# Performance work log

Hardware: AMD Instinct MI355X
Metric: run time of the kernel (lower is better)

## Reference

```python
import jax, jax.numpy as jnp
import numpy as np

D_MODEL = 1024
H = 16
D_K = D_MODEL // H  # 64


def setup_inputs() -> dict:
    key = jax.random.key(0)
    ks = jax.random.split(key, 10)
    s = 1.0 / np.sqrt(D_MODEL)
    x = jax.random.normal(ks[0], (4, 2048, D_MODEL), dtype=jnp.float32)
    # Per-head linear weights stacked: [H, d_model, d_k]
    Wq = jax.random.uniform(ks[1], (H, D_MODEL, D_K), jnp.float32, -s, s)
    bq = jax.random.uniform(ks[2], (H, D_K), jnp.float32, -s, s)
    Wk = jax.random.uniform(ks[3], (H, D_MODEL, D_K), jnp.float32, -s, s)
    bk = jax.random.uniform(ks[4], (H, D_K), jnp.float32, -s, s)
    Wv = jax.random.uniform(ks[5], (H, D_MODEL, D_K), jnp.float32, -s, s)
    bv = jax.random.uniform(ks[6], (H, D_K), jnp.float32, -s, s)
    so = 1.0 / np.sqrt(H * D_K)
    Wo = jax.random.uniform(ks[7], (H * D_K, D_MODEL), jnp.float32, -so, so)
    bo = jax.random.uniform(ks[8], (D_MODEL,), jnp.float32, -so, so)
    return {"x": x, "Wq": Wq, "bq": bq, "Wk": Wk, "bk": bk, "Wv": Wv, "bv": bv, "Wo": Wo, "bo": bo}


def reference(x, Wq, bq, Wk, bk, Wv, bv, Wo, bo):
    # x: [B, S, D]; Wq/Wk/Wv: [H, D, d_k]; b*: [H, d_k]
    q = jnp.einsum('bsd,hdk->bhsk', x, Wq) + bq[None, :, None, :]
    k = jnp.einsum('bsd,hdk->bhsk', x, Wk) + bk[None, :, None, :]
    v = jnp.einsum('bsd,hdk->bhsk', x, Wv) + bv[None, :, None, :]
    scores = jnp.einsum('bhqk,bhsk->bhqs', q, k) / np.sqrt(D_K)
    S = x.shape[1]
    causal = jnp.triu(jnp.ones((S, S), dtype=bool), k=1)  # True above diagonal
    scores = jnp.where(causal, -jnp.inf, scores)
    attn = jax.nn.softmax(scores, axis=-1)
    ctx = jnp.einsum('bhqs,bhsk->bhqk', attn, v)  # [B, H, S, d_k]
    B = x.shape[0]
    # concat heads: torch cats head outputs along last dim -> [B, S, H*d_k]
    ctx = jnp.transpose(ctx, (0, 2, 1, 3)).reshape(B, S, H * D_K)
    return ctx @ Wo + bo
```

## Files before the change

### kernel.cpp

```cpp
#include <hip/hip_runtime.h>
#include <hip/hip_bf16.h>

typedef unsigned short u16;
typedef __attribute__((ext_vector_type(8))) short short8;
typedef __attribute__((ext_vector_type(4))) short short4v;
typedef __attribute__((ext_vector_type(4))) float floatx4;

#define D_MODEL 1024
#define NH 16
#define SEQ 2048
#define BATCH 4
#define M_ROWS 8192
#define N_QKV 3072
#define PS_LD 72

#define QSCALE 0.18033688011112042f
#define EXP2_OFF 11.541560327111707f

__device__ __forceinline__ u16 f2u(float f) {
    __hip_bfloat16 h = __float2bfloat16(f);
    u16 u; __builtin_memcpy(&u, &h, 2); return u;
}

__device__ __forceinline__ void async_copy16(const u16* g, u16* l) {
    __builtin_amdgcn_global_load_lds(
        (const __attribute__((address_space(1))) unsigned int*)(g),
        (__attribute__((address_space(3))) unsigned int*)(l),
        16, 0, 0);
}

__global__ __launch_bounds__(256) void prep(
    const float* __restrict__ x,
    const float* __restrict__ Wq, const float* __restrict__ Wk,
    const float* __restrict__ Wv, const float* __restrict__ Wo,
    const float* __restrict__ bq, const float* __restrict__ bk,
    const float* __restrict__ bv, const float* __restrict__ bo,
    u16* __restrict__ xb, u16* __restrict__ Wpt, u16* __restrict__ Wot,
    float* __restrict__ biasp)
{
    __shared__ u16 T[64 * 72];
    const int tid = threadIdx.x;
    const int blk = blockIdx.x;

    if (blk < 4096) {
        size_t i = ((size_t)blk * 256 + tid) * 8;
        float4 f0 = *(const float4*)&x[i];
        float4 f1 = *(const float4*)&x[i + 4];
        u16 t[8] = {f2u(f0.x), f2u(f0.y), f2u(f0.z), f2u(f0.w),
                    f2u(f1.x), f2u(f1.y), f2u(f1.z), f2u(f1.w)};
        *(short8*)&xb[i] = *(short8*)t;
        return;
    }
    if (blk == 5120) {
        #pragma unroll
        for (int j = 0; j < 16; j++) {
            int idx = j * 256 + tid;
            float v;
            if (idx < 1024)      v = bq[idx] * QSCALE;
            else if (idx < 2048) v = bk[idx - 1024];
            else if (idx < 3072) v = bv[idx - 2048];
            else                 v = bo[idx - 3072];
            biasp[idx] = v;
        }
        return;
    }
    const int wb = blk - 4096;
    const int r = tid >> 2, s4 = (tid & 3) * 16;
    if (wb < 768) {
        int sel = wb / 256, rem = wb % 256;
        int h = rem >> 4, ktile = rem & 15;
        const float* W = (sel == 0) ? Wq : ((sel == 1) ? Wk : Wv);
        const float scale = (sel == 0) ? QSCALE : 1.0f;
        const float* src = W + ((size_t)h * 1024 + ktile * 64 + r) * 64 + s4;
        #pragma unroll
        for (int i = 0; i < 16; i++) T[(s4 + i) * 72 + r] = f2u(src[i] * scale);
        __syncthreads();
        u16 tmp[16];
        #pragma unroll
        for (int i = 0; i < 16; i++) tmp[i] = T[r * 72 + s4 + i];
        u16* dst = Wpt + ((size_t)sel * 1024 + h * 64 + r) * 1024 + ktile * 64 + s4;
        *(short8*)&dst[0] = *(short8*)&tmp[0];
        *(short8*)&dst[8] = *(short8*)&tmp[8];
    } else {
        int rem = wb - 768;
        int nt = rem >> 4, kt2 = rem & 15;
        const float* src = Wo + ((size_t)kt2 * 64 + r) * 1024 + nt * 64 + s4;
        #pragma unroll
        for (int i = 0; i < 16; i++) T[(s4 + i) * 72 + r] = f2u(src[i]);
        __syncthreads();
        u16 tmp[16];
        #pragma unroll
        for (int i = 0; i < 16; i++) tmp[i] = T[r * 72 + s4 + i];
        u16* dst = Wot + ((size_t)nt * 64 + r) * 1024 + kt2 * 64 + s4;
        *(short8*)&dst[0] = *(short8*)&tmp[0];
        *(short8*)&dst[8] = *(short8*)&tmp[8];
    }
}

__global__ __launch_bounds__(256) void vtrans(const u16* __restrict__ QKV,
                                              u16* __restrict__ Vtg) {
    __shared__ u16 T[64 * 72];
    const int bh = blockIdx.x, kt = blockIdx.y;
    const int b = bh >> 4, h = bh & 15;
    const int tid = threadIdx.x;
    const int r = tid >> 2, s4 = (tid & 3) * 16;
    const u16* vp = QKV + (size_t)(b * SEQ + kt * 64 + r) * N_QKV + 2 * D_MODEL + h * 64 + s4;
    *(short8*)&T[r * 72 + s4]     = *(const short8*)&vp[0];
    *(short8*)&T[r * 72 + s4 + 8] = *(const short8*)&vp[8];
    __syncthreads();
    u16 tmp[16];
    #pragma unroll
    for (int i = 0; i < 16; i++) tmp[i] = T[(s4 + i) * 72 + r];
    u16* op = Vtg + ((size_t)bh * 64 + r) * SEQ + kt * 64 + s4;
    *(short8*)&op[0] = *(short8*)&tmp[0];
    *(short8*)&op[8] = *(short8*)&tmp[8];
}

template <typename OT>
__global__ __launch_bounds__(256) void gemm128(
    const u16* __restrict__ A, const u16* __restrict__ Bt,
    const float* __restrict__ bias, OT* __restrict__ C,
    int M, int N, int K)
{
    __shared__ u16 As[128 * 64];
    __shared__ u16 Bs[128 * 64];
    const int tid = threadIdx.x;
    const int w = tid >> 6, lane = tid & 63;
    const int l16 = lane & 15, quad = lane >> 4;

    const int nwgx = gridDim.x;
    const int nwg = nwgx * gridDim.y;
    const int lin = blockIdx.y * nwgx + blockIdx.x;
    const int cpx = nwg >> 3;
    const int swz = (lin & 7) * cpx + (lin >> 3);
    const int bn = (swz % nwgx) * 128, bm = (swz / nwgx) * 128;

    const int wr = (w >> 1) * 64, wc = (w & 1) * 64;

    floatx4 acc[4][4];
    #pragma unroll
    for (int i = 0; i < 4; i++)
        #pragma unroll
        for (int j = 0; j < 4; j++) acc[i][j] = (floatx4){0.f, 0.f, 0.f, 0.f};

    for (int k0 = 0; k0 < K; k0 += 64) {
        #pragma unroll
        for (int c = 0; c < 4; c++) {
            const int off = (w * 4 + c) * 1024 + lane * 16;
            const int row = off >> 7, seg = (off >> 4) & 7;
            async_copy16(A  + (size_t)(bm + row) * K + k0 + seg * 8, &As[(w * 4 + c) * 512]);
            async_copy16(Bt + (size_t)(bn + row) * K + k0 + seg * 8, &Bs[(w * 4 + c) * 512]);
        }
        __syncthreads();
        #pragma unroll
        for (int kc = 0; kc < 2; kc++) {
            short8 a[4], b[4];
            #pragma unroll
            for (int i = 0; i < 4; i++)
                a[i] = *(short8*)&As[(wr + i * 16 + l16) * 64 + kc * 32 + quad * 8];
            #pragma unroll
            for (int i = 0; i < 4; i++)
                b[i] = *(short8*)&Bs[(wc + i * 16 + l16) * 64 + kc * 32 + quad * 8];
            #pragma unroll
            for (int mm = 0; mm < 4; mm++)
                #pragma unroll
                for (int nn = 0; nn < 4; nn++)
                    acc[mm][nn] = __builtin_amdgcn_mfma_f32_16x16x32_bf16(
                        a[mm], b[nn], acc[mm][nn], 0, 0, 0);
        }
        __syncthreads();
    }

    #pragma unroll
    for (int nn = 0; nn < 4; nn++) {
        const int col = bn + wc + nn * 16 + l16;
        const float bi = bias[col];
        #pragma unroll
        for (int mm = 0; mm < 4; mm++) {
            const int row = bm + wr + mm * 16 + quad * 4;
            #pragma unroll
            for (int r = 0; r < 4; r++) {
                float v = acc[mm][nn][r] + bi;
                if constexpr (sizeof(OT) == 2) ((u16*)C)[(size_t)(row + r) * N + col] = f2u(v);
                else                           C[(size_t)(row + r) * N + col] = v;
            }
        }
    }
}

#define G256_BAR   __builtin_amdgcn_s_barrier()
#define G256_LGKM(n) { asm volatile("s_waitcnt lgkmcnt(" #n ")" ::: "memory"); \
                       __builtin_amdgcn_sched_barrier(0); }

#define GQ_STAGE_A(bb, ca, kq) \
    async_copy16(pAc + (size_t)(ca) * 64 * K + (kq), \
                 &lds[(bb) * 28672 + (ca) * 4096 + stw]);

#define GQ_STAGE_B(bb, cb, kq) \
    async_copy16(pBc + (size_t)(cb) * 64 * K + (kq), \
                 &lds[(bb) * 28672 + 16384 + (cb) * 4096 + stw]);

#define GQ_LDA4(dst, bb, mi0) { \
    const int _b = (bb) * 28672 + wm * 8192; \
    _Pragma("unroll") \
    for (int mi = 0; mi < 4; mi++) { \
        const int _r = _b + (((mi0) + mi) * 16 + l16) * 64; \
        dst[mi * 2]     = *(const short8*)&lds[_r + col0]; \
        dst[mi * 2 + 1] = *(const short8*)&lds[_r + col1]; \
    } }

#define GQ_LDB2(dst, bb, ni0) { \
    const int _b = (bb) * 28672 + 16384 + wn * 3072; \
    _Pragma("unroll") \
    for (int ni = 0; ni < 2; ni++) { \
        const int _r = _b + (((ni0) + ni) * 16 + l16) * 64; \
        dst[ni * 2]     = *(const short8*)&lds[_r + col0]; \
        dst[ni * 2 + 1] = *(const short8*)&lds[_r + col1]; \
    } }

#define GQ_LDB1(dst, bb, ni0) { \
    const int _b = (bb) * 28672 + 16384 + wn * 3072; \
    const int _r = _b + ((ni0) * 16 + l16) * 64; \
    dst[0] = *(const short8*)&lds[_r + col0]; \
    dst[1] = *(const short8*)&lds[_r + col1]; }

#define GQ_MMA8(av, bv, MI0, NI0) { \
    _Pragma("unroll") \
    for (int mi = 0; mi < 4; mi++) \
    _Pragma("unroll") \
    for (int ni = 0; ni < 2; ni++) { \
        acc[(MI0) + mi][(NI0) + ni] = __builtin_amdgcn_mfma_f32_16x16x32_bf16( \
            bv[ni * 2],     av[mi * 2],     acc[(MI0) + mi][(NI0) + ni], 0, 0, 0); \
        acc[(MI0) + mi][(NI0) + ni] = __builtin_amdgcn_mfma_f32_16x16x32_bf16( \
            bv[ni * 2 + 1], av[mi * 2 + 1], acc[(MI0) + mi][(NI0) + ni], 0, 0, 0); \
    } }

#define GQ_MMA4(av, bv, MI0) { \
    _Pragma("unroll") \
    for (int mi = 0; mi < 4; mi++) { \
        acc[(MI0) + mi][2] = __builtin_amdgcn_mfma_f32_16x16x32_bf16( \
            bv[0], av[mi * 2],     acc[(MI0) + mi][2], 0, 0, 0); \
        acc[(MI0) + mi][2] = __builtin_amdgcn_mfma_f32_16x16x32_bf16( \
            bv[1], av[mi * 2 + 1], acc[(MI0) + mi][2], 0, 0, 0); \
    } }

template <typename OT>
__global__ __launch_bounds__(512, 2) void gemm_qkv(
    const u16* __restrict__ A, const u16* __restrict__ Bt,
    const float* __restrict__ bias, OT* __restrict__ C,
    int M, int N, int K)
{
    __shared__ u16 lds[57344];
    const int tid = threadIdx.x;
    const int w = tid >> 6, lane = tid & 63;
    const int l16 = lane & 15, quad = lane >> 4;
    const int wm = w >> 2, wn = w & 3;

    const int nwgx = gridDim.x;
    const int nwg = nwgx * gridDim.y;
    const int lin = blockIdx.y * nwgx + blockIdx.x;
    const int cpx = nwg >> 3;
    const int swz = (lin & 7) * cpx + (lin >> 3);
    const int bn = (swz % nwgx) * 192, bm = (swz / nwgx) * 256;

    const int d = tid * 16;
    const int s = d ^ (((d >> 7) & 7) << 4);
    const int r = s >> 7;
    const int c = (s & 127) >> 1;
    const u16* pAc = A  + (size_t)(bm + r) * K + c;
    const u16* pBc = Bt + (size_t)(bn + r) * K + c;
    const int stw = w * 512;

    const int xm = (l16 & 7) << 3;
    const int col0 = (quad * 8) ^ xm;
    const int col1 = (32 + quad * 8) ^ xm;

    floatx4 acc[8][3];
    #pragma unroll
    for (int i = 0; i < 8; i++)
        #pragma unroll
        for (int j = 0; j < 3; j++) acc[i][j] = (floatx4){0.f, 0.f, 0.f, 0.f};

    GQ_STAGE_A(0, 0, 0); GQ_STAGE_A(0, 1, 0); GQ_STAGE_A(0, 2, 0); GQ_STAGE_A(0, 3, 0);
    GQ_STAGE_B(0, 0, 0); GQ_STAGE_B(0, 1, 0); GQ_STAGE_B(0, 2, 0);
    GQ_STAGE_B(1, 0, 64); GQ_STAGE_B(1, 1, 64); GQ_STAGE_B(1, 2, 64);
    asm volatile("s_waitcnt vmcnt(3)" ::: "memory");
    __syncthreads();

    short8 a0[8], a1[8], b0[4], b1[2];
    GQ_LDA4(a0, 0, 0);
    GQ_LDB2(b0, 0, 0);

    const int NKT = K >> 6;
    for (int kt = 0; kt < NKT; ++kt) {
        const int buf = kt & 1, nb = buf ^ 1;
        const int kqA = (kt + 1) << 6, kqB = (kt + 2) << 6;
        const bool st1 = (kt + 1 < NKT), st2 = (kt + 2 < NKT);

        GQ_LDB1(b1, buf, 2);
        if (st1) { GQ_STAGE_A(nb, 0, kqA); GQ_STAGE_A(nb, 1, kqA); }
        G256_BAR; G256_LGKM(2);
        __builtin_amdgcn_s_setprio(1); GQ_MMA8(a0, b0, 0, 0);
        __builtin_amdgcn_s_setprio(0); G256_BAR;

        GQ_LDA4(a1, buf, 4);
        if (st1) { GQ_STAGE_A(nb, 2, kqA); GQ_STAGE_A(nb, 3, kqA); }
        G256_BAR; G256_LGKM(8);
        __builtin_amdgcn_s_setprio(1); GQ_MMA4(a0, b1, 0);
        __builtin_amdgcn_s_setprio(0); G256_BAR;

        if (st2) { GQ_STAGE_B(buf, 0, kqB); GQ_STAGE_B(buf, 1, kqB); }
        G256_BAR; G256_LGKM(0);
        __builtin_amdgcn_s_setprio(1); GQ_MMA8(a1, b0, 4, 0);
        __builtin_amdgcn_s_setprio(0); G256_BAR;

        if (st2) { GQ_STAGE_B(buf, 2, kqB); }
        if (st1) {
            if (st2) { asm volatile("s_waitcnt vmcnt(3)" ::: "memory"); }
            else     { asm volatile("s_waitcnt vmcnt(0)" ::: "memory"); }
            __builtin_amdgcn_sched_barrier(0);
            GQ_LDA4(a0, nb, 0);
            GQ_LDB2(b0, nb, 0);
        }
        G256_BAR;
        __builtin_amdgcn_s_setprio(1); GQ_MMA4(a1, b1, 4);
        __builtin_amdgcn_s_setprio(0); G256_BAR;
    }

    float4 bi[3];
    #pragma unroll
    for (int ni = 0; ni < 3; ni++)
        bi[ni] = *(const float4*)&bias[bn + wn * 48 + ni * 16 + quad * 4];
    #pragma unroll
    for (int mi = 0; mi < 8; mi++) {
        const int row = bm + wm * 128 + mi * 16 + l16;
        #pragma unroll
        for (int ni = 0; ni < 3; ni++) {
            const int col = bn + wn * 48 + ni * 16 + quad * 4;
            const float v0 = acc[mi][ni][0] + bi[ni].x;
            const float v1 = acc[mi][ni][1] + bi[ni].y;
            const float v2 = acc[mi][ni][2] + bi[ni].z;
            const float v3 = acc[mi][ni][3] + bi[ni].w;
            if constexpr (sizeof(OT) == 2) {
                u16 o[4] = {f2u(v0), f2u(v1), f2u(v2), f2u(v3)};
                *(short4v*)&((u16*)C)[(size_t)row * N + col] = *(short4v*)o;
            } else {
                float4 fv = {v0, v1, v2, v3};
                *(float4*)&C[(size_t)row * N + col] = fv;
            }
        }
    }
}

__global__ __launch_bounds__(256) void attn_mfma(
    const u16* __restrict__ QKV, const u16* __restrict__ Vtg, u16* __restrict__ ctx)
{
    __shared__ u16 Ks[2][64 * 64];
    __shared__ u16 Vs[2][64 * 64];
    __shared__ u16 Ps[128 * PS_LD];

    const int bh = blockIdx.x;
    const int qt = (int)(gridDim.y - 1) - (int)blockIdx.y;
    const int b = bh >> 4, h = bh & 15;
    const int tid = threadIdx.x;
    const int w = tid >> 6, lane = tid & 63;
    const int l16 = lane & 15, quad = lane >> 4;

    const int r0 = tid >> 3,        c0 = tid & 7;
    const int r1 = (256 + tid) >> 3, c1 = tid & 7;
    const int sw0 = c0 ^ (r0 & 7), sw1 = c1 ^ (r1 & 7);

    short8 q[2][2];
    #pragma unroll
    for (int m = 0; m < 2; m++) {
        const u16* qp = QKV + (size_t)(b * SEQ + qt * 128 + w * 32 + m * 16 + l16) * N_QKV + h * 64;
        q[m][0] = *(const short8*)&qp[quad * 8];
        q[m][1] = *(const short8*)&qp[32 + quad * 8];
    }

    short8 ones8;
    #pragma unroll
    for (int i = 0; i < 8; i++) ones8[i] = (short)0x3F80;

    floatx4 O[2][4];
    floatx4 lsum[2];
    #pragma unroll
    for (int m = 0; m < 2; m++) {
        lsum[m] = (floatx4){0.f, 0.f, 0.f, 0.f};
        #pragma unroll
        for (int i = 0; i < 4; i++) O[m][i] = (floatx4){0.f, 0.f, 0.f, 0.f};
    }

    const int nkt = 2 * qt + 2;
    const int qrow_w_max = qt * 128 + w * 32 + 31;

    const size_t kbase = (size_t)(b * SEQ) * N_QKV + D_MODEL + h * 64;
    const size_t vbase = (size_t)bh * 64 * SEQ;

    const u16* kpa = QKV + kbase + (size_t)r0 * N_QKV + c0 * 8;
    const u16* kpb = QKV + kbase + (size_t)r1 * N_QKV + c1 * 8;
    const u16* vpa = Vtg + vbase + (size_t)r0 * SEQ + c0 * 8;
    const u16* vpb = Vtg + vbase + (size_t)r1 * SEQ + c1 * 8;

    {
        float4 ka = *(const float4*)kpa;
        float4 kb = *(const float4*)kpb;
        float4 va = *(const float4*)vpa;
        float4 vb = *(const float4*)vpb;
        *(float4*)&Ks[0][r0 * 64 + sw0 * 8] = ka;
        *(float4*)&Ks[0][r1 * 64 + sw1 * 8] = kb;
        *(float4*)&Vs[0][r0 * 64 + sw0 * 8] = va;
        *(float4*)&Vs[0][r1 * 64 + sw1 * 8] = vb;
    }
    kpa += (size_t)64 * N_QKV; kpb += (size_t)64 * N_QKV;
    vpa += 64; vpb += 64;
    __syncthreads();

    for (int kt = 0; kt < nkt; kt++) {
        const int buf = kt & 1;
        const bool pre = (kt + 1 < nkt);
        float4 ka, kb, va, vb;
        if (pre) {
            ka = *(const float4*)kpa;
            kb = *(const float4*)kpb;
            va = *(const float4*)vpa;
            vb = *(const float4*)vpb;
            kpa += (size_t)64 * N_QKV; kpb += (size_t)64 * N_QKV;
            vpa += 64; vpb += 64;
        }

        if (kt * 64 <= qrow_w_max) {
            short8 kf[4][2];
            #pragma unroll
            for (int ns = 0; ns < 4; ns++) {
                const int rr = ns * 16 + l16, rs = rr & 7;
                kf[ns][0] = *(short8*)&Ks[buf][rr * 64 + (quad ^ rs) * 8];
                kf[ns][1] = *(short8*)&Ks[buf][rr * 64 + ((4 + quad) ^ rs) * 8];
            }
            const bool needMask = (kt * 64 + 63 > qt * 128 + w * 32);

            #pragma unroll
            for (int m = 0; m < 2; m++) {
                floatx4 z[4];
                __builtin_amdgcn_s_setprio(1);
                #pragma unroll
                for (int ns = 0; ns < 4; ns++) {
                    floatx4 t = (floatx4){0.f, 0.f, 0.f, 0.f};
                    t = __builtin_amdgcn_mfma_f32_16x16x32_bf16(kf[ns][0], q[m][0], t, 0, 0, 0);
                    t = __builtin_amdgcn_mfma_f32_16x16x32_bf16(kf[ns][1], q[m][1], t, 0, 0, 0);
                    z[ns] = t;
                }
                __builtin_amdgcn_s_setprio(0);
                const int qrow_g = qt * 128 + w * 32 + m * 16 + l16;
                const int prow = (w * 32 + m * 16 + l16) * PS_LD;
                #pragma unroll
                for (int ns = 0; ns < 4; ns++) {
                    u16 pk[4];
                    #pragma unroll
                    for (int r = 0; r < 4; r++) {
                        float s = z[ns][r];
                        const int key = kt * 64 + ns * 16 + quad * 4 + r;
                        if (needMask && key > qrow_g) s = -INFINITY;
                        float p = __builtin_amdgcn_exp2f(s - EXP2_OFF);
                        pk[r] = f2u(p);
                    }
                    *(short4v*)&Ps[prow + ns * 16 + quad * 4] = *(short4v*)pk;
                }
            }

            short8 vf[4][2];
            #pragma unroll
            for (int ds = 0; ds < 4; ds++) {
                const int rr = ds * 16 + l16, rs = rr & 7;
                vf[ds][0] = *(short8*)&Vs[buf][rr * 64 + (quad ^ rs) * 8];
                vf[ds][1] = *(short8*)&Vs[buf][rr * 64 + ((4 + quad) ^ rs) * 8];
            }
            __builtin_amdgcn_s_setprio(1);
            #pragma unroll
            for (int m = 0; m < 2; m++) {
                const int prow = (w * 32 + m * 16 + l16) * PS_LD;
                short8 p0 = *(short8*)&Ps[prow + quad * 8];
                short8 p1 = *(short8*)&Ps[prow + 32 + quad * 8];
                lsum[m] = __builtin_amdgcn_mfma_f32_16x16x32_bf16(ones8, p0, lsum[m], 0, 0, 0);
                lsum[m] = __builtin_amdgcn_mfma_f32_16x16x32_bf16(ones8, p1, lsum[m], 0, 0, 0);
                #pragma unroll
                for (int ds = 0; ds < 4; ds++) {
                    O[m][ds] = __builtin_amdgcn_mfma_f32_16x16x32_bf16(vf[ds][0], p0, O[m][ds], 0, 0, 0);
                    O[m][ds] = __builtin_amdgcn_mfma_f32_16x16x32_bf16(vf[ds][1], p1, O[m][ds], 0, 0, 0);
                }
            }
            __builtin_amdgcn_s_setprio(0);
        }

        if (pre) {
            const int nb = buf ^ 1;
            *(float4*)&Ks[nb][r0 * 64 + sw0 * 8] = ka;
            *(float4*)&Ks[nb][r1 * 64 + sw1 * 8] = kb;
            *(float4*)&Vs[nb][r0 * 64 + sw0 * 8] = va;
            *(float4*)&Vs[nb][r1 * 64 + sw1 * 8] = vb;
        }
        __syncthreads();
    }

    #pragma unroll
    for (int m = 0; m < 2; m++) {
        const float inv = 1.0f / lsum[m][0];
        const size_t base = (size_t)(b * SEQ + qt * 128 + w * 32 + m * 16 + l16) * D_MODEL + h * 64;
        #pragma unroll
        for (int ds = 0; ds < 4; ds++) {
            u16 o[4];
            #pragma unroll
            for (int r = 0; r < 4; r++) o[r] = f2u(O[m][ds][r] * inv);
            *(short4v*)&ctx[base + ds * 16 + quad * 4] = *(short4v*)o;
        }
    }
}

extern "C" void kernel_launch(void* const* d_in, const int* in_sizes, int n_in,
                              void* d_out, int out_size, void* d_ws, size_t ws_size,
                              hipStream_t stream) {
    const float* x  = (const float*)d_in[0];
    const float* Wq = (const float*)d_in[1];
    const float* bq = (const float*)d_in[2];
    const float* Wk = (const float*)d_in[3];
    const float* bk = (const float*)d_in[4];
    const float* Wv = (const float*)d_in[5];
    const float* bv = (const float*)d_in[6];
    const float* Wo = (const float*)d_in[7];
    const float* bo = (const float*)d_in[8];
    float* out = (float*)d_out;

    char* ws = (char*)d_ws;
    float* biasp = (float*)ws;
    u16*   Wpt   = (u16*)(ws + 0x10000);
    u16*   Wot   = (u16*)(ws + 0x620000);
    u16*   xb    = (u16*)(ws + 0x840000);
    u16*   Vtg   = xb;
    u16*   QKV   = (u16*)(ws + 0x1840000);
    u16*   ctx   = (u16*)(ws + 0x4840000);

    prep<<<5121, 256, 0, stream>>>(x, Wq, Wk, Wv, Wo, bq, bk, bv, bo,
                                   xb, Wpt, Wot, biasp);

    gemm_qkv<u16><<<dim3(N_QKV / 192, M_ROWS / 256), 512, 0, stream>>>(
        xb, Wpt, biasp, QKV, M_ROWS, N_QKV, D_MODEL);

    vtrans<<<dim3(64, 32), 256, 0, stream>>>(QKV, Vtg);

    attn_mfma<<<dim3(BATCH * NH, SEQ / 128), 256, 0, stream>>>(QKV, Vtg, ctx);

    gemm128<float><<<dim3(D_MODEL / 128, M_ROWS / 128), 256, 0, stream>>>(
        ctx, Wot, biasp + N_QKV, out, M_ROWS, D_MODEL, D_MODEL);
}
```

Before: 273.7 us.

## Pipeline output GEMM with swizzled double buffer; shrink attention P staging

Replaces the simple output-projection GEMM with a 256x128-tile, 512-thread kernel. It uses XOR-swizzled LDS, double-buffered async global-to-LDS loads and interleaved MFMA phases with priority hints, so loads overlap compute. In attention, all QK^T MFMAs for a tile are issued first. The P staging is then cut to a per-wave 16x64 swizzled LDS buffer reused across the two row groups, which lowers LDS use and allows more waves per CU (launch bounds 4). This adds scheduling complexity and relies on correct vmcnt/lgkmcnt waits for correctness.

Result: slower. 446.1 us (+63.0%).

```diff
diff --git a/kernel.cpp b/kernel.cpp
--- a/kernel.cpp
+++ b/kernel.cpp
@@ -12,7 +12,6 @@
 #define BATCH 4
 #define M_ROWS 8192
 #define N_QKV 3072
-#define PS_LD 72
 
 #define QSCALE 0.18033688011112042f
 #define EXP2_OFF 11.541560327111707f
@@ -114,78 +113,6 @@
     u16* op = Vtg + ((size_t)bh * 64 + r) * SEQ + kt * 64 + s4;
     *(short8*)&op[0] = *(short8*)&tmp[0];
     *(short8*)&op[8] = *(short8*)&tmp[8];
-}
-
-template <typename OT>
-__global__ __launch_bounds__(256) void gemm128(
-    const u16* __restrict__ A, const u16* __restrict__ Bt,
-    const float* __restrict__ bias, OT* __restrict__ C,
-    int M, int N, int K)
-{
-    __shared__ u16 As[128 * 64];
-    __shared__ u16 Bs[128 * 64];
-    const int tid = threadIdx.x;
-    const int w = tid >> 6, lane = tid & 63;
-    const int l16 = lane & 15, quad = lane >> 4;
-
-    const int nwgx = gridDim.x;
-    const int nwg = nwgx * gridDim.y;
-    const int lin = blockIdx.y * nwgx + blockIdx.x;
-    const int cpx = nwg >> 3;
-    const int swz = (lin & 7) * cpx + (lin >> 3);
-    const int bn = (swz % nwgx) * 128, bm = (swz / nwgx) * 128;
-
-    const int wr = (w >> 1) * 64, wc = (w & 1) * 64;
-
-    floatx4 acc[4][4];
-    #pragma unroll
-    for (int i = 0; i < 4; i++)
-        #pragma unroll
-        for (int j = 0; j < 4; j++) acc[i][j] = (floatx4){0.f, 0.f, 0.f, 0.f};
-
-    for (int k0 = 0; k0 < K; k0 += 64) {
-        #pragma unroll
-        for (int c = 0; c < 4; c++) {
-            const int off = (w * 4 + c) * 1024 + lane * 16;
-            const int row = off >> 7, seg = (off >> 4) & 7;
-            async_copy16(A  + (size_t)(bm + row) * K + k0 + seg * 8, &As[(w * 4 + c) * 512]);
-            async_copy16(Bt + (size_t)(bn + row) * K + k0 + seg * 8, &Bs[(w * 4 + c) * 512]);
-        }
-        __syncthreads();
-        #pragma unroll
-        for (int kc = 0; kc < 2; kc++) {
-            short8 a[4], b[4];
-            #pragma unroll
-            for (int i = 0; i < 4; i++)
-                a[i] = *(short8*)&As[(wr + i * 16 + l16) * 64 + kc * 32 + quad * 8];
-            #pragma unroll
-            for (int i = 0; i < 4; i++)
-                b[i] = *(short8*)&Bs[(wc + i * 16 + l16) * 64 + kc * 32 + quad * 8];
-            #pragma unroll
-            for (int mm = 0; mm < 4; mm++)
-                #pragma unroll
-                for (int nn = 0; nn < 4; nn++)
-                    acc[mm][nn] = __builtin_amdgcn_mfma_f32_16x16x32_bf16(
-                        a[mm], b[nn], acc[mm][nn], 0, 0, 0);
-        }
-        __syncthreads();
-    }
-
-    #pragma unroll
-    for (int nn = 0; nn < 4; nn++) {
-        const int col = bn + wc + nn * 16 + l16;
-        const float bi = bias[col];
-        #pragma unroll
-        for (int mm = 0; mm < 4; mm++) {
-            const int row = bm + wr + mm * 16 + quad * 4;
-            #pragma unroll
-            for (int r = 0; r < 4; r++) {
-                float v = acc[mm][nn][r] + bi;
-                if constexpr (sizeof(OT) == 2) ((u16*)C)[(size_t)(row + r) * N + col] = f2u(v);
-                else                           C[(size_t)(row + r) * N + col] = v;
-            }
-        }
-    }
 }
 
 #define G256_BAR   __builtin_amdgcn_s_barrier()
@@ -352,12 +279,142 @@
     }
 }
 
-__global__ __launch_bounds__(256) void attn_mfma(
+#define GO_STAGE_A(bb, ca, kq) \
+    async_copy16(pAc + (size_t)(ca) * 64 * K + (kq), \
+                 &lds[(bb) * 24576 + (ca) * 4096 + stw]);
+
+#define GO_STAGE_B(bb, cb, kq) \
+    async_copy16(pBc + (size_t)(cb) * 64 * K + (kq), \
+                 &lds[(bb) * 24576 + 16384 + (cb) * 4096 + stw]);
+
+#define GO_LDA4(dst, bb, mi0) { \
+    const int _b = (bb) * 24576 + wm * 8192; \
+    _Pragma("unroll") \
+    for (int mi = 0; mi < 4; mi++) { \
+        const int _r = _b + (((mi0) + mi) * 16 + l16) * 64; \
+        dst[mi * 2]     = *(const short8*)&lds[_r + col0]; \
+        dst[mi * 2 + 1] = *(const short8*)&lds[_r + col1]; \
+    } }
+
+#define GO_LDB1(dst, bb, ni) { \
+    const int _b = (bb) * 24576 + 16384; \
+    const int _r = _b + (wn * 32 + (ni) * 16 + l16) * 64; \
+    dst[0] = *(const short8*)&lds[_r + col0]; \
+    dst[1] = *(const short8*)&lds[_r + col1]; }
+
+#define GO_MMA(av, bv, MI0, NI) { \
+    _Pragma("unroll") \
+    for (int mi = 0; mi < 4; mi++) { \
+        acc[(MI0) + mi][NI] = __builtin_amdgcn_mfma_f32_16x16x32_bf16( \
+            bv[0], av[mi * 2],     acc[(MI0) + mi][NI], 0, 0, 0); \
+        acc[(MI0) + mi][NI] = __builtin_amdgcn_mfma_f32_16x16x32_bf16( \
+            bv[1], av[mi * 2 + 1], acc[(MI0) + mi][NI], 0, 0, 0); \
+    } }
+
+__global__ __launch_bounds__(512, 2) void gemm_out(
+    const u16* __restrict__ A, const u16* __restrict__ Bt,
+    const float* __restrict__ bias, float* __restrict__ C,
+    int M, int N, int K)
+{
+    __shared__ u16 lds[49152];
+    const int tid = threadIdx.x;
+    const int w = tid >> 6, lane = tid & 63;
+    const int l16 = lane & 15, quad = lane >> 4;
+    const int wm = w >> 2, wn = w & 3;
+
+    const int nwgx = gridDim.x;
+    const int nwg = nwgx * gridDim.y;
+    const int lin = blockIdx.y * nwgx + blockIdx.x;
+    const int cpx = nwg >> 3;
+    const int swz = (lin & 7) * cpx + (lin >> 3);
+    const int bn = (swz % nwgx) * 128, bm = (swz / nwgx) * 256;
+
+    const int d = tid * 16;
+    const int s = d ^ (((d >> 7) & 7) << 4);
+    const int r = s >> 7;
+    const int c = (s & 127) >> 1;
+    const u16* pAc = A  + (size_t)(bm + r) * K + c;
+    const u16* pBc = Bt + (size_t)(bn + r) * K + c;
+    const int stw = w * 512;
+
+    const int xm = (l16 & 7) << 3;
+    const int col0 = (quad * 8) ^ xm;
+    const int col1 = (32 + quad * 8) ^ xm;
+
+    floatx4 acc[8][2];
+    #pragma unroll
+    for (int i = 0; i < 8; i++)
+        #pragma unroll
+        for (int j = 0; j < 2; j++) acc[i][j] = (floatx4){0.f, 0.f, 0.f, 0.f};
+
+    GO_STAGE_A(0, 0, 0); GO_STAGE_A(0, 1, 0); GO_STAGE_A(0, 2, 0); GO_STAGE_A(0, 3, 0);
+    GO_STAGE_B(0, 0, 0); GO_STAGE_B(0, 1, 0);
+    GO_STAGE_B(1, 0, 64); GO_STAGE_B(1, 1, 64);
+    asm volatile("s_waitcnt vmcnt(2)" ::: "memory");
+    __syncthreads();
+
+    short8 a0[8], a1[8], bb0[2], bb1[2];
+    GO_LDA4(a0, 0, 0);
+    GO_LDB1(bb0, 0, 0);
+
+    const int NKT = K >> 6;
+    for (int kt = 0; kt < NKT; ++kt) {
+        const int buf = kt & 1, nb = buf ^ 1;
+        const int kqA = (kt + 1) << 6, kqB = (kt + 2) << 6;
+        const bool st1 = (kt + 1 < NKT), st2 = (kt + 2 < NKT);
+
+        GO_LDB1(bb1, buf, 1);
+        if (st1) { GO_STAGE_A(nb, 0, kqA); GO_STAGE_A(nb, 1, kqA); }
+        G256_BAR; G256_LGKM(2);
+        __builtin_amdgcn_s_setprio(1); GO_MMA(a0, bb0, 0, 0);
+        __builtin_amdgcn_s_setprio(0); G256_BAR;
+
+        GO_LDA4(a1, buf, 4);
+        if (st1) { GO_STAGE_A(nb, 2, kqA); GO_STAGE_A(nb, 3, kqA); }
+        G256_BAR; G256_LGKM(8);
+        __builtin_amdgcn_s_setprio(1); GO_MMA(a0, bb1, 0, 1);
+        __builtin_amdgcn_s_setprio(0); G256_BAR;
+
+        if (st2) { GO_STAGE_B(buf, 0, kqB); GO_STAGE_B(buf, 1, kqB); }
+        G256_BAR; G256_LGKM(0);
+        __builtin_amdgcn_s_setprio(1); GO_MMA(a1, bb0, 4, 0);
+        __builtin_amdgcn_s_setprio(0); G256_BAR;
+
+        if (st1) {
+            if (st2) { asm volatile("s_waitcnt vmcnt(2)" ::: "memory"); }
+            else     { asm volatile("s_waitcnt vmcnt(0)" ::: "memory"); }
+            __builtin_amdgcn_sched_barrier(0);
+            GO_LDA4(a0, nb, 0);
+            GO_LDB1(bb0, nb, 0);
+        }
+        G256_BAR;
+        __builtin_amdgcn_s_setprio(1); GO_MMA(a1, bb1, 4, 1);
+        __builtin_amdgcn_s_setprio(0); G256_BAR;
+    }
+
+    float4 bi[2];
+    #pragma unroll
+    for (int ni = 0; ni < 2; ni++)
+        bi[ni] = *(const float4*)&bias[bn + wn * 32 + ni * 16 + quad * 4];
+    #pragma unroll
+    for (int mi = 0; mi < 8; mi++) {
+        const int row = bm + wm * 128 + mi * 16 + l16;
+        #pragma unroll
+        for (int ni = 0; ni < 2; ni++) {
+            const int col = bn + wn * 32 + ni * 16 + quad * 4;
+            float4 fv = {acc[mi][ni][0] + bi[ni].x, acc[mi][ni][1] + bi[ni].y,
+                         acc[mi][ni][2] + bi[ni].z, acc[mi][ni][3] + bi[ni].w};
+            *(float4*)&C[(size_t)row * N + col] = fv;
+        }
+    }
+}
+
+__global__ __launch_bounds__(256, 4) void attn_mfma(
     const u16* __restrict__ QKV, const u16* __restrict__ Vtg, u16* __restrict__ ctx)
 {
     __shared__ u16 Ks[2][64 * 64];
     __shared__ u16 Vs[2][64 * 64];
-    __shared__ u16 Ps[128 * PS_LD];
+    __shared__ u16 Ps[4 * 16 * 64];
 
     const int bh = blockIdx.x;
     const int qt = (int)(gridDim.y - 1) - (int)blockIdx.y;
@@ -415,6 +472,9 @@
     kpa += (size_t)64 * N_QKV; kpb += (size_t)64 * N_QKV;
     vpa += 64; vpb += 64;
     __syncthreads();
+
+    const int e7 = l16 & 7;
+    const int pbase = w * 1024 + l16 * 64;
 
     for (int kt = 0; kt < nkt; kt++) {
         const int buf = kt & 1;
@@ -439,34 +499,18 @@
             }
             const bool needMask = (kt * 64 + 63 > qt * 128 + w * 32);
 
+            floatx4 z[2][4];
+            __builtin_amdgcn_s_setprio(1);
             #pragma unroll
-            for (int m = 0; m < 2; m++) {
-                floatx4 z[4];
-                __builtin_amdgcn_s_setprio(1);
+            for (int m = 0; m < 2; m++)
                 #pragma unroll
                 for (int ns = 0; ns < 4; ns++) {
                     floatx4 t = (floatx4){0.f, 0.f, 0.f, 0.f};
                     t = __builtin_amdgcn_mfma_f32_16x16x32_bf16(kf[ns][0], q[m][0], t, 0, 0, 0);
                     t = __builtin_amdgcn_mfma_f32_16x16x32_bf16(kf[ns][1], q[m][1], t, 0, 0, 0);
-                    z[ns] = t;
+                    z[m][ns] = t;
                 }
-                __builtin_amdgcn_s_setprio(0);
-                const int qrow_g = qt * 128 + w * 32 + m * 16 + l16;
-                const int prow = (w * 32 + m * 16 + l16) * PS_LD;
-                #pragma unroll
-                for (int ns = 0; ns < 4; ns++) {
-                    u16 pk[4];
-                    #pragma unroll
-                    for (int r = 0; r < 4; r++) {
-                        float s = z[ns][r];
-                        const int key = kt * 64 + ns * 16 + quad * 4 + r;
-                        if (needMask && key > qrow_g) s = -INFINITY;
-                        float p = __builtin_amdgcn_exp2f(s - EXP2_OFF);
-                        pk[r] = f2u(p);
-                    }
-                    *(short4v*)&Ps[prow + ns * 16 + quad * 4] = *(short4v*)pk;
-                }
-            }
+            __builtin_amdgcn_s_setprio(0);
 
             short8 vf[4][2];
             #pragma unroll
@@ -475,12 +519,26 @@
                 vf[ds][0] = *(short8*)&Vs[buf][rr * 64 + (quad ^ rs) * 8];
                 vf[ds][1] = *(short8*)&Vs[buf][rr * 64 + ((4 + quad) ^ rs) * 8];
             }
-            __builtin_amdgcn_s_setprio(1);
+
             #pragma unroll
             for (int m = 0; m < 2; m++) {
-                const int prow = (w * 32 + m * 16 + l16) * PS_LD;
-                short8 p0 = *(short8*)&Ps[prow + quad * 8];
-                short8 p1 = *(short8*)&Ps[prow + 32 + quad * 8];
+                const int qrow_g = qt * 128 + w * 32 + m * 16 + l16;
+                #pragma unroll
+                for (int ns = 0; ns < 4; ns++) {
+                    u16 pk[4];
+                    #pragma unroll
+                    for (int r = 0; r < 4; r++) {
+                        float s = z[m][ns][r];
+                        const int key = kt * 64 + ns * 16 + quad * 4 + r;
+                        if (needMask && key > qrow_g) s = -INFINITY;
+                        float p = __builtin_amdgcn_exp2f(s - EXP2_OFF);
+                        pk[r] = f2u(p);
+                    }
+                    *(short4v*)&Ps[pbase + (((ns * 4 + quad) ^ (2 * e7)) << 2)] = *(short4v*)pk;
+                }
+                short8 p0 = *(short8*)&Ps[pbase + ((quad ^ e7) << 3)];
+                short8 p1 = *(short8*)&Ps[pbase + (((4 + quad) ^ e7) << 3)];
+                __builtin_amdgcn_s_setprio(1);
                 lsum[m] = __builtin_amdgcn_mfma_f32_16x16x32_bf16(ones8, p0, lsum[m], 0, 0, 0);
                 lsum[m] = __builtin_amdgcn_mfma_f32_16x16x32_bf16(ones8, p1, lsum[m], 0, 0, 0);
                 #pragma unroll
@@ -488,8 +546,8 @@
                     O[m][ds] = __builtin_amdgcn_mfma_f32_16x16x32_bf16(vf[ds][0], p0, O[m][ds], 0, 0, 0);
                     O[m][ds] = __builtin_amdgcn_mfma_f32_16x16x32_bf16(vf[ds][1], p1, O[m][ds], 0, 0, 0);
                 }
+                __builtin_amdgcn_s_setprio(0);
             }
-            __builtin_amdgcn_s_setprio(0);
         }
 
         if (pre) {
@@ -549,6 +607,6 @@
 
     attn_mfma<<<dim3(BATCH * NH, SEQ / 128), 256, 0, stream>>>(QKV, Vtg, ctx);
 
-    gemm128<float><<<dim3(D_MODEL / 128, M_ROWS / 128), 256, 0, stream>>>(
+    gemm_out<<<dim3(D_MODEL / 128, M_ROWS / 256), 512, 0, stream>>>(
         ctx, Wot, biasp + N_QKV, out, M_ROWS, D_MODEL, D_MODEL);
 }
```
